# Kernel tuning notes

Measured on AMD Instinct MI355X. Metric: run time of the kernel, lower is better.

## Reference

```python
import jax, jax.numpy as jnp
import numpy as np

NUM_NODES = 100000
NUM_EDGES = 50000
NUM_CONN = 800000
IN_DIM = 256
HIDDEN = 128
EDGE_ATTR_DIM = 17
LN_EPS = 1e-5


def setup_inputs() -> dict:
    key = jax.random.key(0)
    k1, k2, k3, kw1, kb1, kg, kbeta, kw2, kb2 = jax.random.split(key, 9)
    node_features = jax.random.normal(k1, (NUM_NODES, IN_DIM), dtype=jnp.float32)
    nodes = jax.random.randint(k2, (NUM_CONN,), 0, NUM_NODES, dtype=jnp.int64)
    edges = jax.random.randint(k3, (NUM_CONN,), 0, NUM_EDGES, dtype=jnp.int64)
    hyperedge_index = jnp.stack([nodes, edges], axis=0)
    # MLP params (Linear(in,hid) -> LayerNorm -> ReLU -> Dropout(eval:identity) -> Linear(hid,out))
    W1 = jax.random.normal(kw1, (IN_DIM, HIDDEN), dtype=jnp.float32) * (1.0 / np.sqrt(IN_DIM))
    b1 = jax.random.normal(kb1, (HIDDEN,), dtype=jnp.float32) * 0.01
    ln_g = jnp.ones((HIDDEN,), dtype=jnp.float32)
    ln_b = jnp.zeros((HIDDEN,), dtype=jnp.float32)
    W2 = jax.random.normal(kw2, (HIDDEN, EDGE_ATTR_DIM), dtype=jnp.float32) * (1.0 / np.sqrt(HIDDEN))
    b2 = jax.random.normal(kb2, (EDGE_ATTR_DIM,), dtype=jnp.float32) * 0.01
    return {"node_features": node_features, "hyperedge_index": hyperedge_index,
            "W1": W1, "b1": b1, "ln_g": ln_g, "ln_b": ln_b, "W2": W2, "b2": b2}


def reference(node_features, hyperedge_index, W1, b1, ln_g, ln_b, W2, b2):
    nodes = hyperedge_index[0]
    edges = hyperedge_index[1]
    # indices are in-range by construction (torch valid_mask is all-True here)
    gathered = node_features[nodes]                         # [num_conn, in_dim]
    summed = jax.ops.segment_sum(gathered, edges, num_segments=NUM_EDGES)
    counts = jax.ops.segment_sum(jnp.ones(edges.shape, node_features.dtype), edges,
                                 num_segments=NUM_EDGES)
    edge_features = summed / jnp.clip(counts, 1.0)[:, None]  # mean aggregation
    # decoder MLP (dropout inactive in eval)
    h = edge_features @ W1 + b1
    mu = jnp.mean(h, axis=-1, keepdims=True)
    var = jnp.mean(jnp.square(h - mu), axis=-1, keepdims=True)
    h = (h - mu) * jax.lax.rsqrt(var + LN_EPS) * ln_g + ln_b
    h = jax.nn.relu(h)
    return h @ W2 + b2                                      # [num_edges, edge_attr_dim]
```

## Files before the change

kernel.cpp:

```cpp
#include <hip/hip_runtime.h>
#include <hip/hip_bf16.h>
#include <stdint.h>

#define NUM_NODES 100000
#define NUM_EDGES 50000
#define NUM_CONN  800000
#define IN_DIM    256
#define HIDDEN    128
#define EDGE_DIM  17
#define PAD       64

typedef __bf16 bf16x8 __attribute__((ext_vector_type(8)));
typedef float  f32x4  __attribute__((ext_vector_type(4)));


__global__ void prep_kernel(const float* __restrict__ W1, const float* __restrict__ W2,
                            __bf16* __restrict__ w1f, __bf16* __restrict__ w2f,
                            int* __restrict__ counts) {
    int i = blockIdx.x * 256 + threadIdx.x;
    if (i < NUM_EDGES) counts[i] = 0;
    if (i < 4096) {
        int lane = i & 63, t = (i >> 6) & 7, kc2 = i >> 9;
        int m = lane & 15, q = lane >> 4;
        int n = t * 16 + m;
        int kbase = kc2 * 32 + q * 8;
        __bf16* dst = w1f + (size_t)i * 8;
        #pragma unroll
        for (int ki = 0; ki < 8; ++ki)
            dst[ki] = (__bf16)W1[(size_t)(kbase + ki) * HIDDEN + n];
    } else if (i < 4608) {
        int f = i - 4096;
        int lane = f & 63, t = (f >> 6) & 1, ks = f >> 7;
        int m = lane & 15, q = lane >> 4;
        int n = t * 16 + m;
        int kbase = ks * 32 + q * 8;
        __bf16* dst = w2f + (size_t)f * 8;
        #pragma unroll
        for (int ki = 0; ki < 8; ++ki)
            dst[ki] = (n < EDGE_DIM) ? (__bf16)W2[(size_t)(kbase + ki) * EDGE_DIM + n]
                                     : (__bf16)0.0f;
    }
}

#define FRONT_BLOCKS 1955
__global__ __launch_bounds__(256, 4) void front_kernel(const int* __restrict__ idx,
        int stride, int* __restrict__ counts, int* __restrict__ slots,
        const float* __restrict__ nf, const __bf16* __restrict__ w1f,
        __bf16* __restrict__ pbf) {
    __shared__ __align__(16) __bf16 lds_w[16384];
    const int nb = blockIdx.x / 5, r5 = blockIdx.x % 5;
    if (r5 == 2) {
        long c0 = ((long)nb * 256 + threadIdx.x) * 8;
        if (c0 < NUM_CONN) {
            int nd[8], ed[8];
            if (stride == 2) {
                #pragma unroll
                for (int k = 0; k < 4; ++k) {
                    int4 vn = ((const int4*)idx)[c0 / 2 + k];
                    int4 ve = ((const int4*)(idx + 2 * NUM_CONN))[c0 / 2 + k];
                    nd[2 * k] = vn.x; nd[2 * k + 1] = vn.z;
                    ed[2 * k] = ve.x; ed[2 * k + 1] = ve.z;
                }
            } else {
                #pragma unroll
                for (int k = 0; k < 8; ++k) {
                    nd[k] = idx[c0 + k];
                    ed[k] = idx[NUM_CONN + c0 + k];
                }
            }
            int pos[8];
            #pragma unroll
            for (int k = 0; k < 8; ++k) pos[k] = atomicAdd(&counts[ed[k]], 1);
            #pragma unroll
            for (int k = 0; k < 8; ++k)
                if (pos[k] < PAD) slots[(size_t)ed[k] * PAD + pos[k]] = nd[k];
        }
        return;
    }
    const int p = blockIdx.x - nb - (r5 > 2 ? 1 : 0);
    const int wave = threadIdx.x >> 6;
    const int lane = threadIdx.x & 63;
    const int m = lane & 15, q = lane >> 4;
    int row = p * 64 + wave * 16 + m;
    if (row >= NUM_NODES) row = NUM_NODES - 1;
    const float* ap = nf + (size_t)row * IN_DIM + q * 8;

    const uint4* src = (const uint4*)w1f;
    uint4* dst = (uint4*)lds_w;

    bf16x8 afr[8];
    {
        float4 a4[8];
        #pragma unroll
        for (int kc2 = 0; kc2 < 4; ++kc2) {
            a4[2 * kc2]     = *(const float4*)(ap + kc2 * 32);
            a4[2 * kc2 + 1] = *(const float4*)(ap + kc2 * 32 + 4);
        }
        #pragma unroll
        for (int i = threadIdx.x; i < 2048; i += 256) {
            int kc2 = i >> 8, tt = (i >> 6) & 3, l = i & 63;
            dst[i] = src[(kc2 * 8 + tt) * 64 + l];
        }
        #pragma unroll
        for (int kc2 = 0; kc2 < 4; ++kc2) {
            float4 f0 = a4[2 * kc2], f1 = a4[2 * kc2 + 1];
            afr[kc2][0] = (__bf16)f0.x; afr[kc2][1] = (__bf16)f0.y;
            afr[kc2][2] = (__bf16)f0.z; afr[kc2][3] = (__bf16)f0.w;
            afr[kc2][4] = (__bf16)f1.x; afr[kc2][5] = (__bf16)f1.y;
            afr[kc2][6] = (__bf16)f1.z; afr[kc2][7] = (__bf16)f1.w;
        }
        #pragma unroll
        for (int kc2 = 4; kc2 < 8; ++kc2) {
            a4[2 * (kc2 - 4)]     = *(const float4*)(ap + kc2 * 32);
            a4[2 * (kc2 - 4) + 1] = *(const float4*)(ap + kc2 * 32 + 4);
        }
        #pragma unroll
        for (int kc2 = 4; kc2 < 8; ++kc2) {
            float4 f0 = a4[2 * (kc2 - 4)], f1 = a4[2 * (kc2 - 4) + 1];
            afr[kc2][0] = (__bf16)f0.x; afr[kc2][1] = (__bf16)f0.y;
            afr[kc2][2] = (__bf16)f0.z; afr[kc2][3] = (__bf16)f0.w;
            afr[kc2][4] = (__bf16)f1.x; afr[kc2][5] = (__bf16)f1.y;
            afr[kc2][6] = (__bf16)f1.z; afr[kc2][7] = (__bf16)f1.w;
        }
    }
    __syncthreads();

    const bf16x8* frag = (const bf16x8*)lds_w;
    #pragma unroll
    for (int ph = 0; ph < 2; ++ph) {
        f32x4 acc[4];
        #pragma unroll
        for (int tt = 0; tt < 4; ++tt) acc[tt] = (f32x4){0.f, 0.f, 0.f, 0.f};
        #pragma unroll
        for (int kc2 = 0; kc2 < 8; ++kc2) {
            #pragma unroll
            for (int tt = 0; tt < 4; ++tt)
                acc[tt] = __builtin_amdgcn_mfma_f32_16x16x32_bf16(
                    afr[kc2], frag[(kc2 * 4 + tt) * 64 + lane], acc[tt], 0, 0, 0);
        }
        int ob = p * 64 + wave * 16 + q * 4;
        #pragma unroll
        for (int tt = 0; tt < 4; ++tt) {
            int col = (ph * 4 + tt) * 16 + m;
            #pragma unroll
            for (int r = 0; r < 4; ++r) {
                int orow = ob + r;
                if (orow < NUM_NODES)
                    pbf[(size_t)orow * HIDDEN + col] = (__bf16)acc[tt][r];
            }
        }
        if (ph == 0) {
            __syncthreads();
            #pragma unroll
            for (int i = threadIdx.x; i < 2048; i += 256) {
                int kc2 = i >> 8, tt = (i >> 6) & 3, l = i & 63;
                dst[i] = src[(kc2 * 8 + 4 + tt) * 64 + l];
            }
            __syncthreads();
        }
    }
}

__global__ __launch_bounds__(256) void edge_kernel(const uint4* __restrict__ p4,
        const int* __restrict__ counts, const int* __restrict__ slots,
        const float* __restrict__ b1, const float* __restrict__ ln_g,
        const float* __restrict__ ln_b, const __bf16* __restrict__ w2f,
        const float* __restrict__ b2, float* __restrict__ out) {
    __shared__ __align__(16) uint4 lds_r[256];
    const int wave = threadIdx.x >> 6;
    const int lane = threadIdx.x & 63;
    const int g = lane & 15, ge = lane >> 4;
    const int el = wave * 4 + ge;
    const int e = blockIdx.x * 16 + el;

    const int c = counts[e];
    const int cc = c < PAD ? c : PAD;
    const float inv = 1.0f / (float)(c > 0 ? c : 1);

    float acc[8];
    #pragma unroll
    for (int d = 0; d < 8; ++d) acc[d] = 0.f;

    for (int c0 = 0; c0 < cc; c0 += 16) {
        int slv = slots[(size_t)e * PAD + c0 + g];
        int lim = cc - c0; if (lim > 16) lim = 16;
        if (lim == 16) {
            #pragma unroll
            for (int k0 = 0; k0 < 16; k0 += 4) {
                uint4 u[4];
                #pragma unroll
                for (int k = 0; k < 4; ++k) {
                    int nd = __shfl(slv, ge * 16 + k0 + k, 64);
                    u[k] = p4[(size_t)nd * 16 + g];
                }
                #pragma unroll
                for (int k = 0; k < 4; ++k) {
                    acc[0] += __uint_as_float(u[k].x << 16);
                    acc[1] += __uint_as_float(u[k].x & 0xffff0000u);
                    acc[2] += __uint_as_float(u[k].y << 16);
                    acc[3] += __uint_as_float(u[k].y & 0xffff0000u);
                    acc[4] += __uint_as_float(u[k].z << 16);
                    acc[5] += __uint_as_float(u[k].z & 0xffff0000u);
                    acc[6] += __uint_as_float(u[k].w << 16);
                    acc[7] += __uint_as_float(u[k].w & 0xffff0000u);
                }
            }
        } else {
            for (int k0 = 0; k0 < lim; k0 += 4) {
                uint4 u[4];
                unsigned okm[4];
                #pragma unroll
                for (int k = 0; k < 4; ++k) {
                    int nd = __shfl(slv, ge * 16 + k0 + k, 64);
                    nd = ((unsigned)nd < NUM_NODES) ? nd : 0;
                    u[k] = p4[(size_t)nd * 16 + g];
                    okm[k] = (k0 + k < lim) ? 0xffffffffu : 0u;
                }
                #pragma unroll
                for (int k = 0; k < 4; ++k) {
                    uint4 v = u[k];
                    v.x &= okm[k]; v.y &= okm[k]; v.z &= okm[k]; v.w &= okm[k];
                    acc[0] += __uint_as_float(v.x << 16);
                    acc[1] += __uint_as_float(v.x & 0xffff0000u);
                    acc[2] += __uint_as_float(v.y << 16);
                    acc[3] += __uint_as_float(v.y & 0xffff0000u);
                    acc[4] += __uint_as_float(v.z << 16);
                    acc[5] += __uint_as_float(v.z & 0xffff0000u);
                    acc[6] += __uint_as_float(v.w << 16);
                    acc[7] += __uint_as_float(v.w & 0xffff0000u);
                }
            }
        }
    }

    float4 bA = ((const float4*)b1)[2 * g];
    float4 bB = ((const float4*)b1)[2 * g + 1];
    float h[8];
    h[0] = acc[0] * inv + bA.x; h[1] = acc[1] * inv + bA.y;
    h[2] = acc[2] * inv + bA.z; h[3] = acc[3] * inv + bA.w;
    h[4] = acc[4] * inv + bB.x; h[5] = acc[5] * inv + bB.y;
    h[6] = acc[6] * inv + bB.z; h[7] = acc[7] * inv + bB.w;

    float s = 0.f;
    #pragma unroll
    for (int d = 0; d < 8; ++d) s += h[d];
    #pragma unroll
    for (int off = 8; off > 0; off >>= 1) s += __shfl_xor(s, off, 64);
    float mu = s * (1.0f / 128.0f);

    float dv[8], vv = 0.f;
    #pragma unroll
    for (int d = 0; d < 8; ++d) { dv[d] = h[d] - mu; vv += dv[d] * dv[d]; }
    #pragma unroll
    for (int off = 8; off > 0; off >>= 1) vv += __shfl_xor(vv, off, 64);
    float rs = rsqrtf(vv * (1.0f / 128.0f) + 1e-5f);

    float4 gA = ((const float4*)ln_g)[2 * g];
    float4 gB = ((const float4*)ln_g)[2 * g + 1];
    float4 eA = ((const float4*)ln_b)[2 * g];
    float4 eB = ((const float4*)ln_b)[2 * g + 1];
    float gg[8] = {gA.x, gA.y, gA.z, gA.w, gB.x, gB.y, gB.z, gB.w};
    float ee[8] = {eA.x, eA.y, eA.z, eA.w, eB.x, eB.y, eB.z, eB.w};
    union { __bf16 b[8]; uint4 u; } pk;
    #pragma unroll
    for (int d = 0; d < 8; ++d) {
        float r = dv[d] * rs * gg[d] + ee[d];
        pk.b[d] = (__bf16)(r > 0.f ? r : 0.f);
    }
    lds_r[el * 16 + g] = pk.u;
    __syncthreads();

    if (wave == 0) {
        const int m = lane & 15, q = lane >> 4;
        const __bf16* lr = (const __bf16*)lds_r;
        const bf16x8* fw = (const bf16x8*)w2f;
        f32x4 a0 = (f32x4){0.f, 0.f, 0.f, 0.f};
        f32x4 a1 = (f32x4){0.f, 0.f, 0.f, 0.f};
        #pragma unroll
        for (int ks = 0; ks < 4; ++ks) {
            bf16x8 a = *(const bf16x8*)(lr + m * 128 + ks * 32 + q * 8);
            a0 = __builtin_amdgcn_mfma_f32_16x16x32_bf16(a, fw[(ks * 2 + 0) * 64 + lane], a0, 0, 0, 0);
            a1 = __builtin_amdgcn_mfma_f32_16x16x32_bf16(a, fw[(ks * 2 + 1) * 64 + lane], a1, 0, 0, 0);
        }
        int rowb = blockIdx.x * 16 + q * 4;
        float bm = b2[m];
        float b16 = b2[16];
        #pragma unroll
        for (int r = 0; r < 4; ++r) {
            out[(size_t)(rowb + r) * EDGE_DIM + m] = a0[r] + bm;
            if (m == 0) out[(size_t)(rowb + r) * EDGE_DIM + 16] = a1[r] + b16;
        }
    }
}

extern "C" void kernel_launch(void* const* d_in, const int* in_sizes, int n_in,
                              void* d_out, int out_size, void* d_ws, size_t ws_size,
                              hipStream_t stream) {
    const float* nf  = (const float*)d_in[0];
    const int*   idx = (const int*)d_in[1];
    const float* W1  = (const float*)d_in[2];
    const float* b1  = (const float*)d_in[3];
    const float* g   = (const float*)d_in[4];
    const float* be  = (const float*)d_in[5];
    const float* W2  = (const float*)d_in[6];
    const float* b2  = (const float*)d_in[7];
    float* out = (float*)d_out;

    char* ws = (char*)d_ws;
    __bf16* P      = (__bf16*)ws;
    int*    counts = (int*)(ws + 25600000);
    int*    slots  = (int*)(ws + 25800000);
    __bf16* W1F    = (__bf16*)(ws + 38600000);
    __bf16* W2F    = (__bf16*)(ws + 38665536);

    int stride = (in_sizes[1] == 2 * NUM_CONN) ? 1 : 2;

    prep_kernel<<<196, 256, 0, stream>>>(W1, W2, W1F, W2F, counts);
    front_kernel<<<FRONT_BLOCKS, 256, 0, stream>>>(idx, stride, counts, slots, nf, W1F, P);
    edge_kernel<<<NUM_EDGES / 16, 256, 0, stream>>>((const uint4*)P, counts, slots,
                                                    b1, g, be, W2F, b2, out);
}
```

Measured before the change: 238.5 us.

## Pad edge counters to 64-byte stride and rebalance scatter/GEMM block interleave

Each edge's atomic counter now sits alone in a 64-byte slot (16 ints) instead of being packed, so atomics from different edges no longer share a cache line. The front kernel's block mix changes from 1 scatter block per 4 GEMM blocks to 1 per 2, with each scatter thread handling 4 connections instead of 8. This spreads the atomic work over more blocks and exposes more parallelism. In exchange the counter array grows from 200KB to 3.2MB, the zeroing writes more bytes, and the edge kernel's count reads become strided.

```diff
diff --git a/kernel.cpp b/kernel.cpp
--- a/kernel.cpp
+++ b/kernel.cpp
@@ -9,6 +9,7 @@
 #define HIDDEN    128
 #define EDGE_DIM  17
 #define PAD       64
+#define CSTRIDE   16
 
 typedef __bf16 bf16x8 __attribute__((ext_vector_type(8)));
 typedef float  f32x4  __attribute__((ext_vector_type(4)));
@@ -16,9 +17,13 @@
 
 __global__ void prep_kernel(const float* __restrict__ W1, const float* __restrict__ W2,
                             __bf16* __restrict__ w1f, __bf16* __restrict__ w2f,
-                            int* __restrict__ counts) {
+                            int* __restrict__ counts2) {
     int i = blockIdx.x * 256 + threadIdx.x;
-    if (i < NUM_EDGES) counts[i] = 0;
+    if (i < NUM_EDGES) {
+        int4 z = {0, 0, 0, 0};
+        int4* c4 = (int4*)(counts2 + (size_t)i * CSTRIDE);
+        c4[0] = z; c4[1] = z; c4[2] = z; c4[3] = z;
+    }
     if (i < 4096) {
         int lane = i & 63, t = (i >> 6) & 7, kc2 = i >> 9;
         int m = lane & 15, q = lane >> 4;
@@ -42,20 +47,20 @@
     }
 }
 
-#define FRONT_BLOCKS 1955
+#define FRONT_BLOCKS 2346
 __global__ __launch_bounds__(256, 4) void front_kernel(const int* __restrict__ idx,
-        int stride, int* __restrict__ counts, int* __restrict__ slots,
+        int stride, int* __restrict__ counts2, int* __restrict__ slots,
         const float* __restrict__ nf, const __bf16* __restrict__ w1f,
         __bf16* __restrict__ pbf) {
     __shared__ __align__(16) __bf16 lds_w[16384];
-    const int nb = blockIdx.x / 5, r5 = blockIdx.x % 5;
-    if (r5 == 2) {
-        long c0 = ((long)nb * 256 + threadIdx.x) * 8;
+    const int nb = blockIdx.x / 3, r3 = blockIdx.x % 3;
+    if (r3 == 1) {
+        long c0 = ((long)nb * 256 + threadIdx.x) * 4;
         if (c0 < NUM_CONN) {
-            int nd[8], ed[8];
+            int nd[4], ed[4];
             if (stride == 2) {
                 #pragma unroll
-                for (int k = 0; k < 4; ++k) {
+                for (int k = 0; k < 2; ++k) {
                     int4 vn = ((const int4*)idx)[c0 / 2 + k];
                     int4 ve = ((const int4*)(idx + 2 * NUM_CONN))[c0 / 2 + k];
                     nd[2 * k] = vn.x; nd[2 * k + 1] = vn.z;
@@ -63,21 +68,22 @@
                 }
             } else {
                 #pragma unroll
-                for (int k = 0; k < 8; ++k) {
+                for (int k = 0; k < 4; ++k) {
                     nd[k] = idx[c0 + k];
                     ed[k] = idx[NUM_CONN + c0 + k];
                 }
             }
-            int pos[8];
-            #pragma unroll
-            for (int k = 0; k < 8; ++k) pos[k] = atomicAdd(&counts[ed[k]], 1);
-            #pragma unroll
-            for (int k = 0; k < 8; ++k)
+            int pos[4];
+            #pragma unroll
+            for (int k = 0; k < 4; ++k)
+                pos[k] = atomicAdd(&counts2[(size_t)ed[k] * CSTRIDE], 1);
+            #pragma unroll
+            for (int k = 0; k < 4; ++k)
                 if (pos[k] < PAD) slots[(size_t)ed[k] * PAD + pos[k]] = nd[k];
         }
         return;
     }
-    const int p = blockIdx.x - nb - (r5 > 2 ? 1 : 0);
+    const int p = 2 * nb + (r3 == 2 ? 1 : 0);
     const int wave = threadIdx.x >> 6;
     const int lane = threadIdx.x & 63;
     const int m = lane & 15, q = lane >> 4;
@@ -162,7 +168,7 @@
 }
 
 __global__ __launch_bounds__(256) void edge_kernel(const uint4* __restrict__ p4,
-        const int* __restrict__ counts, const int* __restrict__ slots,
+        const int* __restrict__ counts2, const int* __restrict__ slots,
         const float* __restrict__ b1, const float* __restrict__ ln_g,
         const float* __restrict__ ln_b, const __bf16* __restrict__ w2f,
         const float* __restrict__ b2, float* __restrict__ out) {
@@ -173,7 +179,7 @@
     const int el = wave * 4 + ge;
     const int e = blockIdx.x * 16 + el;
 
-    const int c = counts[e];
+    const int c = counts2[(size_t)e * CSTRIDE];
     const int cc = c < PAD ? c : PAD;
     const float inv = 1.0f / (float)(c > 0 ? c : 1);
 
@@ -307,16 +313,16 @@
     float* out = (float*)d_out;
 
     char* ws = (char*)d_ws;
-    __bf16* P      = (__bf16*)ws;
-    int*    counts = (int*)(ws + 25600000);
-    int*    slots  = (int*)(ws + 25800000);
-    __bf16* W1F    = (__bf16*)(ws + 38600000);
-    __bf16* W2F    = (__bf16*)(ws + 38665536);
+    __bf16* P       = (__bf16*)ws;
+    int*    counts2 = (int*)(ws + 25600000);
+    int*    slots   = (int*)(ws + 28800000);
+    __bf16* W1F     = (__bf16*)(ws + 41600000);
+    __bf16* W2F     = (__bf16*)(ws + 41665536);
 
     int stride = (in_sizes[1] == 2 * NUM_CONN) ? 1 : 2;
 
-    prep_kernel<<<196, 256, 0, stream>>>(W1, W2, W1F, W2F, counts);
-    front_kernel<<<FRONT_BLOCKS, 256, 0, stream>>>(idx, stride, counts, slots, nf, W1F, P);
-    edge_kernel<<<NUM_EDGES / 16, 256, 0, stream>>>((const uint4*)P, counts, slots,
+    prep_kernel<<<196, 256, 0, stream>>>(W1, W2, W1F, W2F, counts2);
+    front_kernel<<<FRONT_BLOCKS, 256, 0, stream>>>(idx, stride, counts2, slots, nf, W1F, P);
+    edge_kernel<<<NUM_EDGES / 16, 256, 0, stream>>>((const uint4*)P, counts2, slots,
                                                     b1, g, be, W2F, b2, out);
 }
```

Result: no change. 234.8 us (-1.6%).
